# Optimization experiments

Measured on AMD Instinct MI355X. Metric: run time of the kernel, lower is better.

Reference implementation:

```python
import jax, jax.numpy as jnp
import numpy as np

B, S, K, F = 256, 512, 32, 64
H1, H2 = 512, 256


def setup_inputs() -> dict:
    key = jax.random.key(0)
    ks = jax.random.split(key, 8)
    x = jax.random.normal(ks[0], (B, S, F), dtype=jnp.float32)
    neighborhood = jax.random.randint(ks[1], (S, K), 0, S)
    distances = jax.random.uniform(ks[2], (S, K), dtype=jnp.float32)
    in_w = K * (F + 1)  # 2080
    W1 = jax.random.normal(ks[3], (in_w, H1), dtype=jnp.float32) * 0.02
    b1 = jnp.zeros((H1,), dtype=jnp.float32)
    W2 = jax.random.normal(ks[4], (H1, H2), dtype=jnp.float32) * 0.02
    b2 = jnp.zeros((H2,), dtype=jnp.float32)
    Wd = jax.random.normal(ks[5], (H2, 1), dtype=jnp.float32) * 0.02
    bd = jnp.zeros((1,), dtype=jnp.float32)
    return {"x": x, "neighborhood": neighborhood, "distances": distances,
            "W1": W1, "b1": b1, "W2": W2, "b2": b2, "Wd": Wd, "bd": bd}


def reference(x, neighborhood, distances, W1, b1, W2, b2, Wd, bd):
    b, s, f = x.shape
    k = neighborhood.shape[1]
    # make_k_tensor: gather neighbors and append per-edge distance
    gathered = x[:, neighborhood, :]                      # [B, S, K, F]
    dist = jnp.broadcast_to(distances[None, :, :, None], (b, s, k, 1))
    kt = jnp.concatenate([gathered, dist], axis=-1)        # [B, S, K, F+1]
    # filter phase: shared MLP over flattened neighborhoods
    flat = kt.reshape(b * s, k * (f + 1))                  # [B*S, K*(F+1)]
    h = jax.nn.relu(flat @ W1 + b1)
    h = h @ W2 + b2                                        # [B*S, H2]
    h = h.reshape(b, s, -1)
    # max pool over sequence, then final dense
    m = jnp.max(h, axis=1)                                 # [B, H2]
    out = jax.nn.relu(m) @ Wd + bd                         # [B, 1]
    return out.squeeze(1)                                  # [B]
```

## Files before the change

kernel.cpp:

```cpp
#include <hip/hip_runtime.h>

typedef __attribute__((ext_vector_type(8))) short short8;
typedef __attribute__((ext_vector_type(4))) float f32x4;

constexpr int Bb = 256, Ss = 512, Kk = 32, Ff = 64, H1 = 512, H2 = 256;
constexpr int Mtot = Bb * Ss;
constexpr int Mh = Mtot / 2;
constexpr int KD1 = Kk * Ff;

#define DEVI static __device__ __forceinline__

DEVI unsigned short f2b(float f) {
  unsigned u = __float_as_uint(f);
  return (unsigned short)((u + 0x7FFFu + ((u >> 16) & 1u)) >> 16);
}

DEVI void stage16(const void* g, void* l) {
  __builtin_amdgcn_global_load_lds((const __attribute__((address_space(1))) void*)g,
                                   (__attribute__((address_space(3))) void*)l, 16, 0, 0);
}

__global__ void k_cvt_x(const float* __restrict__ x, unsigned short* __restrict__ xbf) {
  int i = blockIdx.x * 256 + threadIdx.x;
  float4 v = ((const float4*)x)[i];
  ushort4 o;
  o.x = f2b(v.x); o.y = f2b(v.y); o.z = f2b(v.z); o.w = f2b(v.w);
  ((ushort4*)xbf)[i] = o;
}

__global__ void k_w1t(const float* __restrict__ W1, unsigned short* __restrict__ w1t) {
  int idx = blockIdx.x * 256 + threadIdx.x;
  int h = idx >> 11, i = idx & 2047;
  int k = i >> 6, f = i & 63;
  w1t[idx] = f2b(W1[(k * 65 + f) * 512 + h]);
}

__global__ void k_w2t(const float* __restrict__ W2, unsigned short* __restrict__ w2t) {
  int idx = blockIdx.x * 256 + threadIdx.x;
  int n = idx >> 9, k = idx & 511;
  w2t[idx] = f2b(W2[k * 256 + n]);
}

__global__ void k_dbias(const float* __restrict__ W1, const float* __restrict__ b1,
                        const float* __restrict__ dist, float* __restrict__ dbias) {
  int idx = blockIdx.x * 256 + threadIdx.x;
  int s = idx >> 9, h = idx & 511;
  float a = b1[h];
  #pragma unroll
  for (int k = 0; k < 32; ++k)
    a += dist[s * 32 + k] * W1[(k * 65 + 64) * 512 + h];
  dbias[idx] = a;
}


__global__ __launch_bounds__(256, 2) void k_gemm1(
    const unsigned short* __restrict__ xbf, const unsigned short* __restrict__ w1t,
    const int* __restrict__ nb, const float* __restrict__ dbias,
    unsigned short* __restrict__ h1, int mbase) {
  __shared__ __align__(16) unsigned short As[128 * 64];
  __shared__ __align__(16) unsigned short Bs[128 * 64];
  const int tid = threadIdx.x;
  const int lane = tid & 63;
  const int w = tid >> 6;
  const int wm = w >> 1, wn = w & 1;
  const int mblk = blockIdx.x >> 2;
  const int nblk = blockIdx.x & 3;
  const int r0l = mblk << 7;
  const int r0g = mbase + r0l;
  const int b = r0g >> 9;
  const int s0 = r0g & 511;
  const int ncol0 = nblk << 7;
  const int arow = lane >> 3;
  const int scol = (((lane & 7) ^ (lane >> 3)) << 3);

  f32x4 acc[4][4];
  #pragma unroll
  for (int m = 0; m < 4; ++m)
    #pragma unroll
    for (int n = 0; n < 4; ++n) acc[m][n] = (f32x4){0.f, 0.f, 0.f, 0.f};

  for (int t = 0; t < 32; ++t) {
    #pragma unroll
    for (int i = 0; i < 4; ++i) {
      int rr = (w << 5) + (i << 3);
      int row = rr + arow;
      int j = nb[((s0 + row) << 5) + t];
      stage16(xbf + (((size_t)((b << 9) + j)) << 6) + scol, As + rr * 64);
    }
    #pragma unroll
    for (int i = 0; i < 4; ++i) {
      int rr = (w << 5) + (i << 3);
      int row = rr + arow;
      stage16(w1t + (((size_t)(ncol0 + row)) << 11) + (t << 6) + scol, Bs + rr * 64);
    }
    asm volatile("s_waitcnt vmcnt(0)" ::: "memory");
    __syncthreads();
    #pragma unroll
    for (int ks = 0; ks < 2; ++ks) {
      const int rdoff = ((((ks << 2) + (lane >> 4)) ^ (lane & 7)) << 3);
      short8 af[4], bfr[4];
      #pragma unroll
      for (int m = 0; m < 4; ++m)
        af[m] = *(const short8*)(As + ((wm << 6) + (m << 4) + (lane & 15)) * 64 + rdoff);
      #pragma unroll
      for (int n = 0; n < 4; ++n)
        bfr[n] = *(const short8*)(Bs + ((wn << 6) + (n << 4) + (lane & 15)) * 64 + rdoff);
      #pragma unroll
      for (int m = 0; m < 4; ++m)
        #pragma unroll
        for (int n = 0; n < 4; ++n)
          acc[m][n] = __builtin_amdgcn_mfma_f32_16x16x32_bf16(af[m], bfr[n], acc[m][n], 0, 0, 0);
    }
    __syncthreads();
  }

  #pragma unroll
  for (int m = 0; m < 4; ++m) {
    int rowl = (wm << 6) + (m << 4) + ((lane >> 4) << 2);
    #pragma unroll
    for (int n = 0; n < 4; ++n) {
      int col = ncol0 + (wn << 6) + (n << 4) + (lane & 15);
      #pragma unroll
      for (int r = 0; r < 4; ++r) {
        int rowL = r0l + rowl + r;
        float v = acc[m][n][r] + dbias[(((r0g + rowl + r) & 511) << 9) + col];
        v = v > 0.f ? v : 0.f;
        h1[((size_t)rowL << 9) + col] = f2b(v);
      }
    }
  }
}

__global__ __launch_bounds__(256, 2) void k_gemm2(
    const unsigned short* __restrict__ h1, const unsigned short* __restrict__ w2t,
    const float* __restrict__ b2, unsigned* __restrict__ mrelu, int mbase) {
  __shared__ __align__(16) unsigned short As[128 * 64];
  __shared__ __align__(16) unsigned short Bs[128 * 64];
  const int tid = threadIdx.x;
  const int lane = tid & 63;
  const int w = tid >> 6;
  const int wm = w >> 1, wn = w & 1;
  const int mblk = blockIdx.x >> 1;
  const int nblk = blockIdx.x & 1;
  const int r0l = mblk << 7;
  const int b = (mbase + r0l) >> 9;
  const int ncol0 = nblk << 7;
  const int arow = lane >> 3;
  const int scol = (((lane & 7) ^ (lane >> 3)) << 3);

  f32x4 acc[4][4];
  #pragma unroll
  for (int m = 0; m < 4; ++m)
    #pragma unroll
    for (int n = 0; n < 4; ++n) acc[m][n] = (f32x4){0.f, 0.f, 0.f, 0.f};

  for (int t = 0; t < 8; ++t) {
    #pragma unroll
    for (int i = 0; i < 4; ++i) {
      int rr = (w << 5) + (i << 3);
      int row = rr + arow;
      stage16(h1 + (((size_t)(r0l + row)) << 9) + (t << 6) + scol, As + rr * 64);
      stage16(w2t + (((size_t)(ncol0 + row)) << 9) + (t << 6) + scol, Bs + rr * 64);
    }
    asm volatile("s_waitcnt vmcnt(0)" ::: "memory");
    __syncthreads();
    #pragma unroll
    for (int ks = 0; ks < 2; ++ks) {
      const int rdoff = ((((ks << 2) + (lane >> 4)) ^ (lane & 7)) << 3);
      short8 af[4], bfr[4];
      #pragma unroll
      for (int m = 0; m < 4; ++m)
        af[m] = *(const short8*)(As + ((wm << 6) + (m << 4) + (lane & 15)) * 64 + rdoff);
      #pragma unroll
      for (int n = 0; n < 4; ++n)
        bfr[n] = *(const short8*)(Bs + ((wn << 6) + (n << 4) + (lane & 15)) * 64 + rdoff);
      #pragma unroll
      for (int m = 0; m < 4; ++m)
        #pragma unroll
        for (int n = 0; n < 4; ++n)
          acc[m][n] = __builtin_amdgcn_mfma_f32_16x16x32_bf16(af[m], bfr[n], acc[m][n], 0, 0, 0);
    }
    __syncthreads();
  }

  #pragma unroll
  for (int n = 0; n < 4; ++n) {
    int col = ncol0 + (wn << 6) + (n << 4) + (lane & 15);
    float cm = -1e30f;
    #pragma unroll
    for (int m = 0; m < 4; ++m)
      #pragma unroll
      for (int r = 0; r < 4; ++r) cm = fmaxf(cm, acc[m][n][r]);
    cm = fmaxf(cm, __shfl_xor(cm, 16));
    cm = fmaxf(cm, __shfl_xor(cm, 32));
    if ((lane >> 4) == 0) {
      float v = fmaxf(cm + b2[col], 0.f);
      atomicMax(mrelu + ((b << 8) + col), __float_as_uint(v));
    }
  }
}

__global__ void k_final(const unsigned* __restrict__ mrelu, const float* __restrict__ wd,
                        const float* __restrict__ bd, float* __restrict__ out) {
  int b = blockIdx.x, t = threadIdx.x;
  float v = __uint_as_float(mrelu[(b << 8) + t]) * wd[t];
  #pragma unroll
  for (int o = 32; o > 0; o >>= 1) v += __shfl_down(v, o);
  __shared__ float p[4];
  if ((t & 63) == 0) p[t >> 6] = v;
  __syncthreads();
  if (t == 0) out[b] = p[0] + p[1] + p[2] + p[3] + bd[0];
}

extern "C" void kernel_launch(void* const* d_in, const int* in_sizes, int n_in,
                              void* d_out, int out_size, void* d_ws, size_t ws_size,
                              hipStream_t stream) {
  (void)in_sizes; (void)n_in; (void)out_size; (void)ws_size;
  const float* x    = (const float*)d_in[0];
  const int*   nb   = (const int*)d_in[1];
  const float* dist = (const float*)d_in[2];
  const float* W1   = (const float*)d_in[3];
  const float* b1   = (const float*)d_in[4];
  const float* W2   = (const float*)d_in[5];
  const float* b2   = (const float*)d_in[6];
  const float* Wd   = (const float*)d_in[7];
  const float* bd   = (const float*)d_in[8];
  float* out = (float*)d_out;

  char* p = (char*)d_ws;
  unsigned short* xbf   = (unsigned short*)p; p += (size_t)Bb * Ss * Ff * 2;
  unsigned short* w1t   = (unsigned short*)p; p += (size_t)H1 * KD1 * 2;
  unsigned short* w2t   = (unsigned short*)p; p += (size_t)H2 * H1 * 2;
  float*          dbias = (float*)p;          p += (size_t)Ss * H1 * 4;
  unsigned*       mrelu = (unsigned*)p;       p += (size_t)Bb * H2 * 4;
  unsigned short* h1    = (unsigned short*)p; p += (size_t)Mh * H1 * 2;

  hipMemsetAsync(mrelu, 0, (size_t)Bb * H2 * 4, stream);
  k_cvt_x<<<(Bb * Ss * Ff / 4) / 256, 256, 0, stream>>>(x, xbf);
  k_w1t<<<(H1 * KD1) / 256, 256, 0, stream>>>(W1, w1t);
  k_w2t<<<(H2 * H1) / 256, 256, 0, stream>>>(W2, w2t);
  k_dbias<<<(Ss * H1) / 256, 256, 0, stream>>>(W1, b1, dist, dbias);
  for (int hh = 0; hh < 2; ++hh) {
    int mbase = hh * Mh;
    k_gemm1<<<(Mh / 128) * (H1 / 128), 256, 0, stream>>>(xbf, w1t, nb, dbias, h1, mbase);
    k_gemm2<<<(Mh / 128) * (H2 / 128), 256, 0, stream>>>(h1, w2t, b2, mrelu, mbase);
  }
  k_final<<<Bb, 256, 0, stream>>>(mrelu, Wd, bd, out);
}
```

Before: 442.8 us.

## Double-buffer gather GEMM1 with 256x256 tiles and widen GEMM2 to full N

GEMM1 moves to 512-thread blocks with 256x256 output tiles and double-buffered LDS. Loads for the next K step are interleaved with MFMA phases, separated by raw s_barrier, and the MFMA phases run at raised wave priority. Neighbor indices are prefetched two steps ahead. GEMM2 now has each block cover all 256 output columns for 128 rows, which halves the atomics and re-reads of h1. The cost is more registers (128 accumulator floats per lane) and 128KB of LDS per GEMM1 block, which may limit occupancy.

```diff
diff --git a/kernel.cpp b/kernel.cpp
--- a/kernel.cpp
+++ b/kernel.cpp
@@ -9,6 +9,8 @@
 constexpr int KD1 = Kk * Ff;
 
 #define DEVI static __device__ __forceinline__
+#define BARRIER asm volatile("s_barrier" ::: "memory")
+#define VMCNT(N) asm volatile("s_waitcnt vmcnt(" #N ")" ::: "memory")
 
 DEVI unsigned short f2b(float f) {
   unsigned u = __float_as_uint(f);
@@ -53,79 +55,130 @@
 }
 
 
-__global__ __launch_bounds__(256, 2) void k_gemm1(
+__global__ __launch_bounds__(512, 2) void k_gemm1(
     const unsigned short* __restrict__ xbf, const unsigned short* __restrict__ w1t,
     const int* __restrict__ nb, const float* __restrict__ dbias,
     unsigned short* __restrict__ h1, int mbase) {
-  __shared__ __align__(16) unsigned short As[128 * 64];
-  __shared__ __align__(16) unsigned short Bs[128 * 64];
+  __shared__ __align__(16) unsigned short lds[2][2][256 * 64];
   const int tid = threadIdx.x;
   const int lane = tid & 63;
   const int w = tid >> 6;
-  const int wm = w >> 1, wn = w & 1;
-  const int mblk = blockIdx.x >> 2;
-  const int nblk = blockIdx.x & 3;
-  const int r0l = mblk << 7;
+  const int wm = w >> 2, wn = w & 3;
+  const int mblk = blockIdx.x >> 1;
+  const int nblk = blockIdx.x & 1;
+  const int r0l = mblk << 8;
   const int r0g = mbase + r0l;
   const int b = r0g >> 9;
   const int s0 = r0g & 511;
-  const int ncol0 = nblk << 7;
-  const int arow = lane >> 3;
-  const int scol = (((lane & 7) ^ (lane >> 3)) << 3);
-
-  f32x4 acc[4][4];
-  #pragma unroll
-  for (int m = 0; m < 4; ++m)
+  const int ncol0 = nblk << 8;
+  const int scol8 = (((lane & 7) ^ ((lane >> 3) & 7)) << 3);
+
+  int nbi[4];
+  #pragma unroll
+  for (int u = 0; u < 4; ++u)
+    nbi[u] = (s0 + (u << 6) + (w << 3) + (lane >> 3)) << 5;
+
+  f32x4 acc[8][4];
+  #pragma unroll
+  for (int m = 0; m < 8; ++m)
     #pragma unroll
     for (int n = 0; n < 4; ++n) acc[m][n] = (f32x4){0.f, 0.f, 0.f, 0.f};
 
+  #pragma unroll
+  for (int u = 0; u < 4; ++u) {
+    int j = nb[nbi[u]];
+    stage16(xbf + (((size_t)((b << 9) + j)) << 6) + scol8,
+            &lds[0][0][(u << 12) + (w << 9)]);
+  }
+  #pragma unroll
+  for (int u = 0; u < 4; ++u)
+    stage16(w1t + (((size_t)(ncol0 + (u << 6) + (w << 3) + (lane >> 3))) << 11) + scol8,
+            &lds[0][1][(u << 12) + (w << 9)]);
+  int j4[4];
+  #pragma unroll
+  for (int u = 0; u < 4; ++u) j4[u] = nb[nbi[u] + 1];
+  VMCNT(0);
+  BARRIER;
+
   for (int t = 0; t < 32; ++t) {
-    #pragma unroll
-    for (int i = 0; i < 4; ++i) {
-      int rr = (w << 5) + (i << 3);
-      int row = rr + arow;
-      int j = nb[((s0 + row) << 5) + t];
-      stage16(xbf + (((size_t)((b << 9) + j)) << 6) + scol, As + rr * 64);
+    unsigned short* As = &lds[t & 1][0][0];
+    unsigned short* Bs = &lds[t & 1][1][0];
+    unsigned short* An = &lds[(t & 1) ^ 1][0][0];
+    unsigned short* Bn = &lds[(t & 1) ^ 1][1][0];
+    const bool pf = (t < 31);
+    short8 a[4], bq[4];
+    int jn[4];
+
+#define RD_A(mq, ks)                                                             \
+    _Pragma("unroll")                                                            \
+    for (int i = 0; i < 4; ++i)                                                  \
+      a[i] = *(const short8*)(As + ((wm << 7) + ((mq) << 6) + (i << 4) +         \
+               (lane & 15)) * 64 + (((((ks) << 2) + (lane >> 4)) ^ (lane & 7)) << 3));
+#define RD_B(ks)                                                                 \
+    _Pragma("unroll")                                                            \
+    for (int n = 0; n < 4; ++n)                                                  \
+      bq[n] = *(const short8*)(Bs + ((wn << 6) + (n << 4) + (lane & 15)) * 64 +  \
+               (((((ks) << 2) + (lane >> 4)) ^ (lane & 7)) << 3));
+#define STA(u) stage16(xbf + (((size_t)((b << 9) + j4[u])) << 6) + scol8,        \
+                       An + ((u) << 12) + (w << 9))
+#define STB(u) stage16(w1t + (((size_t)(ncol0 + ((u) << 6) + (w << 3) +          \
+                       (lane >> 3))) << 11) + ((t + 1) << 6) + scol8,            \
+                       Bn + ((u) << 12) + (w << 9))
+#define MM(mq)                                                                   \
+    _Pragma("unroll")                                                            \
+    for (int i = 0; i < 4; ++i)                                                  \
+      _Pragma("unroll")                                                          \
+      for (int n = 0; n < 4; ++n)                                                \
+        acc[((mq) << 2) + i][n] = __builtin_amdgcn_mfma_f32_16x16x32_bf16(       \
+            a[i], bq[n], acc[((mq) << 2) + i][n], 0, 0, 0);
+
+    RD_A(0, 0); RD_B(0);
+    if (pf) { STA(0); STA(2); VMCNT(2); } else { VMCNT(0); }
+    BARRIER;
+    __builtin_amdgcn_s_setprio(1); MM(0); __builtin_amdgcn_s_setprio(0);
+    BARRIER;
+    RD_A(1, 0);
+    if (pf) { STB(0); STB(1); }
+    BARRIER;
+    __builtin_amdgcn_s_setprio(1); MM(1); __builtin_amdgcn_s_setprio(0);
+    BARRIER;
+    RD_A(0, 1); RD_B(1);
+    {
+      int tt = (t + 2 < 32) ? (t + 2) : 31;
+      #pragma unroll
+      for (int u = 0; u < 4; ++u) jn[u] = nb[nbi[u] + tt];
     }
-    #pragma unroll
-    for (int i = 0; i < 4; ++i) {
-      int rr = (w << 5) + (i << 3);
-      int row = rr + arow;
-      stage16(w1t + (((size_t)(ncol0 + row)) << 11) + (t << 6) + scol, Bs + rr * 64);
-    }
-    asm volatile("s_waitcnt vmcnt(0)" ::: "memory");
-    __syncthreads();
-    #pragma unroll
-    for (int ks = 0; ks < 2; ++ks) {
-      const int rdoff = ((((ks << 2) + (lane >> 4)) ^ (lane & 7)) << 3);
-      short8 af[4], bfr[4];
-      #pragma unroll
-      for (int m = 0; m < 4; ++m)
-        af[m] = *(const short8*)(As + ((wm << 6) + (m << 4) + (lane & 15)) * 64 + rdoff);
-      #pragma unroll
-      for (int n = 0; n < 4; ++n)
-        bfr[n] = *(const short8*)(Bs + ((wn << 6) + (n << 4) + (lane & 15)) * 64 + rdoff);
-      #pragma unroll
-      for (int m = 0; m < 4; ++m)
-        #pragma unroll
-        for (int n = 0; n < 4; ++n)
-          acc[m][n] = __builtin_amdgcn_mfma_f32_16x16x32_bf16(af[m], bfr[n], acc[m][n], 0, 0, 0);
-    }
-    __syncthreads();
-  }
-
-  #pragma unroll
-  for (int m = 0; m < 4; ++m) {
-    int rowl = (wm << 6) + (m << 4) + ((lane >> 4) << 2);
+    if (pf) { STB(2); STB(3); }
+    BARRIER;
+    __builtin_amdgcn_s_setprio(1); MM(0); __builtin_amdgcn_s_setprio(0);
+    BARRIER;
+    RD_A(1, 1);
+    if (pf) { STA(1); STA(3); VMCNT(2); }
+    BARRIER;
+    __builtin_amdgcn_s_setprio(1); MM(1); __builtin_amdgcn_s_setprio(0);
+    BARRIER;
+
+    #pragma unroll
+    for (int u = 0; u < 4; ++u) j4[u] = jn[u];
+#undef RD_A
+#undef RD_B
+#undef STA
+#undef STB
+#undef MM
+  }
+
+  #pragma unroll
+  for (int fm = 0; fm < 8; ++fm) {
+    int rowl = (wm << 7) + (fm << 4) + ((lane >> 4) << 2);
     #pragma unroll
     for (int n = 0; n < 4; ++n) {
       int col = ncol0 + (wn << 6) + (n << 4) + (lane & 15);
       #pragma unroll
       for (int r = 0; r < 4; ++r) {
-        int rowL = r0l + rowl + r;
-        float v = acc[m][n][r] + dbias[(((r0g + rowl + r) & 511) << 9) + col];
+        int rl = rowl + r;
+        float v = acc[fm][n][r] + dbias[((((r0g + rl) & 511)) << 9) + col];
         v = v > 0.f ? v : 0.f;
-        h1[((size_t)rowL << 9) + col] = f2b(v);
+        h1[((size_t)(r0l + rl) << 9) + col] = f2b(v);
       }
     }
   }
@@ -135,62 +188,60 @@
     const unsigned short* __restrict__ h1, const unsigned short* __restrict__ w2t,
     const float* __restrict__ b2, unsigned* __restrict__ mrelu, int mbase) {
   __shared__ __align__(16) unsigned short As[128 * 64];
-  __shared__ __align__(16) unsigned short Bs[128 * 64];
+  __shared__ __align__(16) unsigned short Bs[256 * 64];
   const int tid = threadIdx.x;
   const int lane = tid & 63;
   const int w = tid >> 6;
-  const int wm = w >> 1, wn = w & 1;
-  const int mblk = blockIdx.x >> 1;
-  const int nblk = blockIdx.x & 1;
-  const int r0l = mblk << 7;
+  const int r0l = blockIdx.x << 7;
   const int b = (mbase + r0l) >> 9;
-  const int ncol0 = nblk << 7;
-  const int arow = lane >> 3;
-  const int scol = (((lane & 7) ^ (lane >> 3)) << 3);
-
-  f32x4 acc[4][4];
-  #pragma unroll
-  for (int m = 0; m < 4; ++m)
+  const int scol8 = (((lane & 7) ^ ((lane >> 3) & 7)) << 3);
+
+  f32x4 acc[8][4];
+  #pragma unroll
+  for (int m = 0; m < 8; ++m)
     #pragma unroll
     for (int n = 0; n < 4; ++n) acc[m][n] = (f32x4){0.f, 0.f, 0.f, 0.f};
 
   for (int t = 0; t < 8; ++t) {
     #pragma unroll
-    for (int i = 0; i < 4; ++i) {
-      int rr = (w << 5) + (i << 3);
-      int row = rr + arow;
-      stage16(h1 + (((size_t)(r0l + row)) << 9) + (t << 6) + scol, As + rr * 64);
-      stage16(w2t + (((size_t)(ncol0 + row)) << 9) + (t << 6) + scol, Bs + rr * 64);
-    }
-    asm volatile("s_waitcnt vmcnt(0)" ::: "memory");
+    for (int a2 = 0; a2 < 4; ++a2)
+      stage16(h1 + (((size_t)(r0l + (w << 5) + (a2 << 3) + (lane >> 3))) << 9) +
+                  (t << 6) + scol8,
+              As + (w << 11) + (a2 << 9));
+    #pragma unroll
+    for (int b2i = 0; b2i < 8; ++b2i)
+      stage16(w2t + (((size_t)((w << 6) + (b2i << 3) + (lane >> 3))) << 9) +
+                  (t << 6) + scol8,
+              Bs + (w << 12) + (b2i << 9));
+    VMCNT(0);
     __syncthreads();
     #pragma unroll
     for (int ks = 0; ks < 2; ++ks) {
       const int rdoff = ((((ks << 2) + (lane >> 4)) ^ (lane & 7)) << 3);
-      short8 af[4], bfr[4];
-      #pragma unroll
-      for (int m = 0; m < 4; ++m)
-        af[m] = *(const short8*)(As + ((wm << 6) + (m << 4) + (lane & 15)) * 64 + rdoff);
+      short8 af[8], bf[4];
+      #pragma unroll
+      for (int fm = 0; fm < 8; ++fm)
+        af[fm] = *(const short8*)(As + ((fm << 4) + (lane & 15)) * 64 + rdoff);
       #pragma unroll
       for (int n = 0; n < 4; ++n)
-        bfr[n] = *(const short8*)(Bs + ((wn << 6) + (n << 4) + (lane & 15)) * 64 + rdoff);
-      #pragma unroll
-      for (int m = 0; m < 4; ++m)
+        bf[n] = *(const short8*)(Bs + ((w << 6) + (n << 4) + (lane & 15)) * 64 + rdoff);
+      #pragma unroll
+      for (int fm = 0; fm < 8; ++fm)
         #pragma unroll
         for (int n = 0; n < 4; ++n)
-          acc[m][n] = __builtin_amdgcn_mfma_f32_16x16x32_bf16(af[m], bfr[n], acc[m][n], 0, 0, 0);
+          acc[fm][n] = __builtin_amdgcn_mfma_f32_16x16x32_bf16(af[fm], bf[n], acc[fm][n], 0, 0, 0);
     }
     __syncthreads();
   }
 
   #pragma unroll
   for (int n = 0; n < 4; ++n) {
-    int col = ncol0 + (wn << 6) + (n << 4) + (lane & 15);
+    int col = (w << 6) + (n << 4) + (lane & 15);
     float cm = -1e30f;
     #pragma unroll
-    for (int m = 0; m < 4; ++m)
-      #pragma unroll
-      for (int r = 0; r < 4; ++r) cm = fmaxf(cm, acc[m][n][r]);
+    for (int fm = 0; fm < 8; ++fm)
+      #pragma unroll
+      for (int r = 0; r < 4; ++r) cm = fmaxf(cm, acc[fm][n][r]);
     cm = fmaxf(cm, __shfl_xor(cm, 16));
     cm = fmaxf(cm, __shfl_xor(cm, 32));
     if ((lane >> 4) == 0) {
@@ -242,8 +293,8 @@
   k_dbias<<<(Ss * H1) / 256, 256, 0, stream>>>(W1, b1, dist, dbias);
   for (int hh = 0; hh < 2; ++hh) {
     int mbase = hh * Mh;
-    k_gemm1<<<(Mh / 128) * (H1 / 128), 256, 0, stream>>>(xbf, w1t, nb, dbias, h1, mbase);
-    k_gemm2<<<(Mh / 128) * (H2 / 128), 256, 0, stream>>>(h1, w2t, b2, mrelu, mbase);
+    k_gemm1<<<(Mh / 256) * (H1 / 256), 512, 0, stream>>>(xbf, w1t, nb, dbias, h1, mbase);
+    k_gemm2<<<(Mh / 128), 256, 0, stream>>>(h1, w2t, b2, mrelu, mbase);
   }
   k_final<<<Bb, 256, 0, stream>>>(mrelu, Wd, bd, out);
 }
```

Measured after the change: 408.7 us. -7.7%, faster.
